# Kernel optimization log

Measured on AMD Instinct MI355X. Metric: run time of the kernel, lower is better.

## Reference

```python
import jax, jax.numpy as jnp
import numpy as np

D_IN = 2048
D_OUT = 2048
NUM_HEADS = 16
HEAD_DIM = D_OUT // NUM_HEADS


def setup_inputs() -> dict:
    key = jax.random.key(0)
    k_x, k_qkv, k_proj, k_b = jax.random.split(key, 4)
    x = jax.random.normal(k_x, (2, 2048, D_IN), dtype=jnp.float32)
    # torch Linear(d_in, 3*d_out, bias=False): weight [3*d_out, d_in]; store transposed [d_in, 3*d_out]
    Wqkv = jax.random.normal(k_qkv, (D_IN, 3 * D_OUT), dtype=jnp.float32) / np.sqrt(D_IN)
    Wproj = jax.random.normal(k_proj, (D_OUT, D_OUT), dtype=jnp.float32) / np.sqrt(D_OUT)
    bproj = jax.random.normal(k_b, (D_OUT,), dtype=jnp.float32) * 0.01
    return {"x": x, "Wqkv": Wqkv, "Wproj": Wproj, "bproj": bproj}


def reference(x, Wqkv, Wproj, bproj):
    B, S, _ = x.shape
    qkv = x @ Wqkv  # [B, S, 3*D_OUT]
    qkv = qkv.reshape(B, S, 3, NUM_HEADS, HEAD_DIM)
    qkv = jnp.transpose(qkv, (2, 0, 3, 1, 4))  # [3, B, H, S, Dh]
    q, k, v = qkv[0], qkv[1], qkv[2]
    scale = 1.0 / np.sqrt(HEAD_DIM).astype(np.float32)
    scores = jnp.einsum('bhqd,bhkd->bhqk', q, k) * scale  # [B, H, S, S]
    causal = jnp.tril(jnp.ones((S, S), dtype=bool))
    scores = jnp.where(causal, scores, jnp.finfo(scores.dtype).min)
    attn = jax.nn.softmax(scores, axis=-1)
    out = jnp.einsum('bhqk,bhkd->bhqd', attn, v)  # [B, H, S, Dh]
    out = jnp.transpose(out, (0, 2, 1, 3)).reshape(B, S, D_OUT)
    return out @ Wproj + bproj
```

## Files before the change

### kernel.cpp

```cpp
#include <hip/hip_runtime.h>
#include <stdint.h>

typedef __attribute__((ext_vector_type(8))) short short8;
typedef __attribute__((ext_vector_type(4))) float f32x4;
typedef __attribute__((ext_vector_type(16))) float f32x16;
typedef __attribute__((ext_vector_type(4))) unsigned short u16x4;

typedef unsigned short u16;

constexpr int S_LEN = 2048;
constexpr int DH    = 128;

__device__ __forceinline__ u16 f2bf(float f) {
    union { float f; unsigned u; } v; v.f = f;
    unsigned r = v.u + 0x7FFFu + ((v.u >> 16) & 1u);
    return (u16)(r >> 16);
}
__device__ __forceinline__ void gl_lds16(const void* g, void* l) {
    __builtin_amdgcn_global_load_lds((const __attribute__((address_space(1))) void*)g,
                                     (__attribute__((address_space(3))) void*)l,
                                     16, 0, 0);
}

__global__ __launch_bounds__(256) void convx(const float* __restrict__ src,
                                             u16* __restrict__ dst) {
    size_t i = ((size_t)blockIdx.x * 256 + threadIdx.x) * 8;
    f32x4 a = *(const f32x4*)(src + i);
    f32x4 b = *(const f32x4*)(src + i + 4);
    short8 r;
    r[0] = (short)f2bf(a[0]); r[1] = (short)f2bf(a[1]);
    r[2] = (short)f2bf(a[2]); r[3] = (short)f2bf(a[3]);
    r[4] = (short)f2bf(b[0]); r[5] = (short)f2bf(b[1]);
    r[6] = (short)f2bf(b[2]); r[7] = (short)f2bf(b[3]);
    *(short8*)(dst + i) = r;
}

__global__ __launch_bounds__(256) void convT(const float* __restrict__ src,
                                             u16* __restrict__ dst,
                                             int rows, int cols) {
    __shared__ u16 t[64][65];
    const int c0 = blockIdx.x * 64, r0 = blockIdx.y * 64;
    const int tid = threadIdx.x;
    const int colq = (tid & 15) * 4;
    const int rw   = tid >> 4;
#pragma unroll
    for (int p = 0; p < 4; ++p) {
        int row = p * 16 + rw;
        f32x4 v = *(const f32x4*)(src + (size_t)(r0 + row) * cols + c0 + colq);
        t[colq + 0][row] = f2bf(v[0]);
        t[colq + 1][row] = f2bf(v[1]);
        t[colq + 2][row] = f2bf(v[2]);
        t[colq + 3][row] = f2bf(v[3]);
    }
    __syncthreads();
    const int rowq = (tid & 15) * 4;
    const int cw   = tid >> 4;
#pragma unroll
    for (int p = 0; p < 4; ++p) {
        int col = p * 16 + cw;
        u16x4 o;
        o[0] = t[col][rowq + 0]; o[1] = t[col][rowq + 1];
        o[2] = t[col][rowq + 2]; o[3] = t[col][rowq + 3];
        *(u16x4*)(dst + (size_t)(c0 + col) * rows + r0 + rowq) = o;
    }
}

__global__ __launch_bounds__(512, 2) void gemm_qkv(
        const u16* __restrict__ A, const u16* __restrict__ BT,
        u16* __restrict__ Qo, u16* __restrict__ Ko, u16* __restrict__ VTo) {
    __shared__ __align__(16) u16 lA[2][128 * 64];
    __shared__ __align__(16) u16 lB[2][256 * 64];
    const int tid = threadIdx.x;
    const int lane = tid & 63, wave = tid >> 6;
    const int quad = lane >> 4, l16 = lane & 15;
    const int wr = wave >> 2, wc = wave & 3;
    const int m0 = blockIdx.y * 128, n0 = blockIdx.x * 256;
    const int sw = l16 & 7;
    const int c4 = tid & 7;
    f32x4 acc[4][4] = {};

    auto stageA = [&](int t1, int nb) {
#pragma unroll
        for (int j = 0; j < 2; ++j) {
            int idx = j * 512 + tid;
            int row = idx >> 3;
            gl_lds16(A + (size_t)(m0 + row) * 2048 + t1 * 64 + ((c4 ^ (row & 7)) * 8),
                     &lA[nb][row * 64 + c4 * 8]);
        }
    };
    auto stageB = [&](int h, int t1, int nb) {
#pragma unroll
        for (int j = 0; j < 2; ++j) {
            int rih = (j * 512 + tid) >> 3;
            int row = (rih & 31) + h * 32 + (rih >> 5) * 64;
            gl_lds16(BT + (size_t)(n0 + row) * 2048 + t1 * 64 + ((c4 ^ (row & 7)) * 8),
                     &lB[nb][row * 64 + c4 * 8]);
        }
    };

    stageA(0, 0); stageB(0, 0, 0); stageB(1, 0, 0);

    constexpr int NT = 32;
    for (int t = 0; t < NT; ++t) {
        const int buf = t & 1, nb = buf ^ 1;
        const bool pf = (t + 1 < NT);
        asm volatile("s_waitcnt vmcnt(2)\n\ts_barrier" ::: "memory");
        short8 af[4][2], bf0[2][2];
        const int abase = (wr * 64 + l16) * 64;
        const int bbase = (wc * 64 + l16) * 64;
#pragma unroll
        for (int m = 0; m < 4; ++m)
#pragma unroll
            for (int ks = 0; ks < 2; ++ks)
                af[m][ks] = *(const short8*)&lA[buf][abase + m * 1024 + (((ks * 4 + quad) ^ sw)) * 8];
#pragma unroll
        for (int n = 0; n < 2; ++n)
#pragma unroll
            for (int ks = 0; ks < 2; ++ks)
                bf0[n][ks] = *(const short8*)&lB[buf][bbase + n * 1024 + (((ks * 4 + quad) ^ sw)) * 8];
        if (pf) { stageA(t + 1, nb); stageB(0, t + 1, nb); }
        __builtin_amdgcn_s_setprio(1);
#pragma unroll
        for (int m = 0; m < 4; ++m)
#pragma unroll
            for (int n = 0; n < 2; ++n)
#pragma unroll
                for (int ks = 0; ks < 2; ++ks)
                    acc[m][n] = __builtin_amdgcn_mfma_f32_16x16x32_bf16(
                        af[m][ks], bf0[n][ks], acc[m][n], 0, 0, 0);
        __builtin_amdgcn_s_setprio(0);
        if (pf) asm volatile("s_waitcnt vmcnt(4)\n\ts_barrier" ::: "memory");
        else    asm volatile("s_waitcnt vmcnt(0)\n\ts_barrier" ::: "memory");
        short8 bf1[2][2];
#pragma unroll
        for (int n = 0; n < 2; ++n)
#pragma unroll
            for (int ks = 0; ks < 2; ++ks)
                bf1[n][ks] = *(const short8*)&lB[buf][bbase + 2048 + n * 1024 + (((ks * 4 + quad) ^ sw)) * 8];
        if (pf) stageB(1, t + 1, nb);
        __builtin_amdgcn_s_setprio(1);
#pragma unroll
        for (int m = 0; m < 4; ++m)
#pragma unroll
            for (int n = 0; n < 2; ++n)
#pragma unroll
                for (int ks = 0; ks < 2; ++ks)
                    acc[m][n + 2] = __builtin_amdgcn_mfma_f32_16x16x32_bf16(
                        af[m][ks], bf1[n][ks], acc[m][n + 2], 0, 0, 0);
        __builtin_amdgcn_s_setprio(0);
    }

#pragma unroll
    for (int m = 0; m < 4; ++m) {
        int r0r = m0 + wr * 64 + m * 16 + quad * 4;
        int b = r0r >> 11, s0 = r0r & 2047;
#pragma unroll
        for (int n = 0; n < 4; ++n) {
            int cc = n0 + wc * 64 + n * 16 + l16;
            int which = cc >> 11, hd = (cc >> 7) & 15, dh = cc & 127;
            if (which < 2) {
                u16* dst = which == 0 ? Qo : Ko;
#pragma unroll
                for (int rg = 0; rg < 4; ++rg)
                    dst[(size_t)((b * 16 + hd) * 2048 + s0 + rg) * 128 + dh] = f2bf(acc[m][n][rg]);
            } else {
                u16x4 v;
#pragma unroll
                for (int rg = 0; rg < 4; ++rg) v[rg] = f2bf(acc[m][n][rg]);
                *(u16x4*)&VTo[((size_t)(b * 16 + hd) * 128 + dh) * 2048 + s0] = v;
            }
        }
    }
}

__global__ __launch_bounds__(256, 2) void attn_kern(
        u16* __restrict__ QOp, const u16* __restrict__ Kp,
        const u16* __restrict__ VTp) {
    __shared__ __align__(16) u16 lK[2][64 * 128];
    __shared__ __align__(16) u16 lV[2][128 * 64];
    const int tid = threadIdx.x, lane = tid & 63, wave = tid >> 6;
    const int ql = lane & 31, hi = lane >> 5;
    const int qb = (blockIdx.y < 8) ? (15 - (int)blockIdx.y) : ((int)blockIdx.y - 8);
    const int bh = blockIdx.x;
    const int qbase = qb * 128 + wave * 32;
    const int qmax = qbase + 31;
    const int nkt = 2 * qb + 2;
    u16* Qh = QOp + (size_t)bh * S_LEN * DH;
    const u16* Kh = Kp + (size_t)bh * S_LEN * DH;
    const u16* VTh = VTp + (size_t)bh * DH * S_LEN;

    short8 qf[8];
#pragma unroll
    for (int c = 0; c < 8; ++c)
        qf[c] = *(const short8*)&Qh[(size_t)(qbase + ql) * 128 + c * 16 + hi * 8];

    f32x16 acc[4] = {};
    float mrun = -1e30f, lrun = 0.f;
    const float SC = 0.08838834764831845f * 1.44269504088896f;

    auto stageK = [&](int kt, int b) {
        const u16* ks = Kh + (size_t)kt * 64 * 128;
#pragma unroll
        for (int p = 0; p < 4; ++p) {
            int slot = p * 256 + tid;
            int row = slot >> 4, c4 = slot & 15;
            gl_lds16(ks + row * 128 + ((c4 ^ (row & 15)) * 8), &lK[b][slot * 8]);
        }
    };
    auto stageV = [&](int kt, int b) {
        const u16* vs = VTh + kt * 64;
#pragma unroll
        for (int p = 0; p < 4; ++p) {
            int slot = p * 256 + tid;
            int row = slot >> 3, c4 = slot & 7;
            gl_lds16(vs + (size_t)row * 2048 + ((c4 ^ (row & 7)) * 8), &lV[b][slot * 8]);
        }
    };

    stageK(0, 0);
    stageV(0, 0);
    asm volatile("s_waitcnt vmcnt(4)\n\ts_barrier" ::: "memory");

    for (int kt = 0; kt < nkt; ++kt) {
        const int buf = kt & 1;
        const bool more = kt + 1 < nkt;
        const bool compute = (kt * 64 <= qmax);
        float pv0[16], pv1[16];
        if (compute) {
            const bool part = (kt * 64 + 63 > qbase);
            f32x16 s0 = {}, s1 = {};
            __builtin_amdgcn_s_setprio(1);
#pragma unroll
            for (int c = 0; c < 8; ++c) {
                int sl = ((c * 2 + hi) ^ (ql & 15)) * 8;
                short8 k0 = *(const short8*)&lK[buf][ql * 128 + sl];
                short8 k1 = *(const short8*)&lK[buf][(32 + ql) * 128 + sl];
                s0 = __builtin_amdgcn_mfma_f32_32x32x16_bf16(k0, qf[c], s0, 0, 0, 0);
                s1 = __builtin_amdgcn_mfma_f32_32x32x16_bf16(k1, qf[c], s1, 0, 0, 0);
            }
            __builtin_amdgcn_s_setprio(0);
            if (more) stageK(kt + 1, buf ^ 1);
            float pm = -1e30f;
            const int qg = qbase + ql;
#pragma unroll
            for (int r = 0; r < 16; ++r) {
                int krow = (r & 3) + 8 * (r >> 2) + 4 * hi;
                float a = s0[r] * SC;
                float b = s1[r] * SC;
                if (part) {
                    if (kt * 64 + krow > qg)      a = -1e30f;
                    if (kt * 64 + 32 + krow > qg) b = -1e30f;
                }
                pv0[r] = a; pv1[r] = b;
                pm = fmaxf(pm, fmaxf(a, b));
            }
            pm = fmaxf(pm, __shfl_xor(pm, 32));
            if (__any(pm - mrun > 8.f)) {
                float mn = fmaxf(mrun, pm);
                float al = exp2f(mrun - mn);
                mrun = mn;
                lrun *= al;
#pragma unroll
                for (int r = 0; r < 16; ++r) {
                    float ar = __shfl(al, (r & 3) + 8 * (r >> 2) + 4 * hi);
#pragma unroll
                    for (int dc = 0; dc < 4; ++dc)
                        acc[dc][r] *= ar;
                }
            }
            float rs = 0.f;
#pragma unroll
            for (int r = 0; r < 16; ++r) {
                pv0[r] = exp2f(pv0[r] - mrun);
                pv1[r] = exp2f(pv1[r] - mrun);
                rs += pv0[r] + pv1[r];
            }
            rs += __shfl_xor(rs, 32);
            lrun += rs;
        } else if (more) {
            stageK(kt + 1, buf ^ 1);
        }
        if (more) asm volatile("s_waitcnt vmcnt(4)\n\ts_barrier" ::: "memory");
        else      asm volatile("s_waitcnt vmcnt(0)\n\ts_barrier" ::: "memory");
        if (compute) {
            unsigned X0[8], X1[8];
#pragma unroll
            for (int i = 0; i < 8; ++i) {
                X0[i] = (unsigned)f2bf(pv0[2 * i]) | ((unsigned)f2bf(pv0[2 * i + 1]) << 16);
                X1[i] = (unsigned)f2bf(pv1[2 * i]) | ((unsigned)f2bf(pv1[2 * i + 1]) << 16);
            }
            short8 pa[4];
#pragma unroll
            for (int t = 0; t < 2; ++t)
#pragma unroll
                for (int h = 0; h < 2; ++h) {
                    unsigned x0 = t ? X1[4 * h + 0] : X0[4 * h + 0];
                    unsigned x1 = t ? X1[4 * h + 1] : X0[4 * h + 1];
                    unsigned x2 = t ? X1[4 * h + 2] : X0[4 * h + 2];
                    unsigned x3 = t ? X1[4 * h + 3] : X0[4 * h + 3];
                    unsigned sx0 = (unsigned)__shfl_xor((int)x0, 32);
                    unsigned sx1 = (unsigned)__shfl_xor((int)x1, 32);
                    unsigned sx2 = (unsigned)__shfl_xor((int)x2, 32);
                    unsigned sx3 = (unsigned)__shfl_xor((int)x3, 32);
                    union { unsigned u[4]; short8 s; } uf;
                    uf.u[0] = hi ? sx2 : x0;
                    uf.u[1] = hi ? sx3 : x1;
                    uf.u[2] = hi ? x2 : sx0;
                    uf.u[3] = hi ? x3 : sx1;
                    pa[t * 2 + h] = uf.s;
                }
            __builtin_amdgcn_s_setprio(1);
#pragma unroll
            for (int dc = 0; dc < 4; ++dc) {
                const int rv = dc * 32 + ql;
#pragma unroll
                for (int kc = 0; kc < 4; ++kc) {
                    short8 vf = *(const short8*)&lV[buf][rv * 64 + (((kc * 2 + hi) ^ (ql & 7)) * 8)];
                    acc[dc] = __builtin_amdgcn_mfma_f32_32x32x16_bf16(pa[kc], vf, acc[dc], 0, 0, 0);
                }
            }
            __builtin_amdgcn_s_setprio(0);
        }
        if (more) {
            stageV(kt + 1, buf ^ 1);
            asm volatile("s_waitcnt vmcnt(4)\n\ts_barrier" ::: "memory");
        }
    }

    float linv = 1.f / lrun;
#pragma unroll
    for (int r = 0; r < 16; ++r) {
        int qr = (r & 3) + 8 * (r >> 2) + 4 * hi;
        float lr = __shfl(linv, qr);
        int qq = qbase + qr;
#pragma unroll
        for (int dc = 0; dc < 4; ++dc)
            Qh[(size_t)qq * 128 + dc * 32 + ql] = f2bf(acc[dc][r] * lr);
    }
}

__global__ __launch_bounds__(256, 2) void gemm_proj(
        const u16* __restrict__ QO, const u16* __restrict__ BT,
        const float* __restrict__ bias, float* __restrict__ out) {
    __shared__ __align__(16) u16 lA[2][128 * 64];
    __shared__ __align__(16) u16 lB[2][128 * 64];
    const int tid = threadIdx.x;
    const int lane = tid & 63, wave = tid >> 6;
    const int quad = lane >> 4, l16 = lane & 15;
    const int wm = wave >> 1, wn = wave & 1;
    const int bid = blockIdx.x;
    const int swz = (bid & 7) * 64 + (bid >> 3);
    const int m0 = (swz >> 4) * 128, n0 = (swz & 15) * 128;
    const int sw = l16 & 7;
    const int c4 = tid & 7;
    f32x4 acc[4][4] = {};

    auto stageA = [&](int t1, int nb) {
#pragma unroll
        for (int j = 0; j < 4; ++j) {
            int row = (j * 256 + tid) >> 3;
            int r = m0 + row;
            int b = r >> 11, s = r & 2047;
            int k = t1 * 64 + ((c4 ^ (row & 7)) * 8);
            int h = k >> 7, dh = k & 127;
            gl_lds16(QO + ((size_t)(b * 16 + h) * 2048 + s) * 128 + dh,
                     &lA[nb][row * 64 + c4 * 8]);
        }
    };
    auto stageB = [&](int h, int t1, int nb) {
#pragma unroll
        for (int j = 0; j < 2; ++j) {
            int rih = (j * 256 + tid) >> 3;
            int row = (rih & 31) + h * 32 + (rih >> 5) * 64;
            gl_lds16(BT + (size_t)(n0 + row) * 2048 + t1 * 64 + ((c4 ^ (row & 7)) * 8),
                     &lB[nb][row * 64 + c4 * 8]);
        }
    };

    stageB(0, 0, 0);
    asm volatile("" ::: "memory");
    stageA(0, 0);
    asm volatile("" ::: "memory");
    stageB(1, 0, 0);

    constexpr int NT = 32;
    for (int t = 0; t < NT; ++t) {
        const int buf = t & 1, nb = buf ^ 1;
        const bool pf = (t + 1 < NT);
        asm volatile("s_waitcnt vmcnt(2)\n\ts_barrier" ::: "memory");
        short8 af[4][2], bf0[2][2];
        const int abase = (wm * 64 + l16) * 64;
        const int bbase = (wn * 64 + l16) * 64;
#pragma unroll
        for (int m = 0; m < 4; ++m)
#pragma unroll
            for (int ks = 0; ks < 2; ++ks)
                af[m][ks] = *(const short8*)&lA[buf][abase + m * 1024 + (((ks * 4 + quad) ^ sw)) * 8];
#pragma unroll
        for (int n = 0; n < 2; ++n)
#pragma unroll
            for (int ks = 0; ks < 2; ++ks)
                bf0[n][ks] = *(const short8*)&lB[buf][bbase + n * 1024 + (((ks * 4 + quad) ^ sw)) * 8];
        if (pf) {
            stageB(0, t + 1, nb);
            asm volatile("" ::: "memory");
            stageA(t + 1, nb);
        }
        __builtin_amdgcn_s_setprio(1);
#pragma unroll
        for (int m = 0; m < 4; ++m)
#pragma unroll
            for (int n = 0; n < 2; ++n)
#pragma unroll
                for (int ks = 0; ks < 2; ++ks)
                    acc[m][n] = __builtin_amdgcn_mfma_f32_16x16x32_bf16(
                        af[m][ks], bf0[n][ks], acc[m][n], 0, 0, 0);
        __builtin_amdgcn_s_setprio(0);
        if (pf) asm volatile("s_waitcnt vmcnt(6)\n\ts_barrier" ::: "memory");
        else    asm volatile("s_waitcnt vmcnt(0)\n\ts_barrier" ::: "memory");
        short8 bf1[2][2];
#pragma unroll
        for (int n = 0; n < 2; ++n)
#pragma unroll
            for (int ks = 0; ks < 2; ++ks)
                bf1[n][ks] = *(const short8*)&lB[buf][bbase + 2048 + n * 1024 + (((ks * 4 + quad) ^ sw)) * 8];
        if (pf) stageB(1, t + 1, nb);
        __builtin_amdgcn_s_setprio(1);
#pragma unroll
        for (int m = 0; m < 4; ++m)
#pragma unroll
            for (int n = 0; n < 2; ++n)
#pragma unroll
                for (int ks = 0; ks < 2; ++ks)
                    acc[m][n + 2] = __builtin_amdgcn_mfma_f32_16x16x32_bf16(
                        af[m][ks], bf1[n][ks], acc[m][n + 2], 0, 0, 0);
        __builtin_amdgcn_s_setprio(0);
    }

#pragma unroll
    for (int m = 0; m < 4; ++m) {
        int r0r = m0 + wm * 64 + m * 16 + quad * 4;
#pragma unroll
        for (int n = 0; n < 4; ++n) {
            int cc = n0 + wn * 64 + n * 16 + l16;
            float bv = bias[cc];
#pragma unroll
            for (int rg = 0; rg < 4; ++rg)
                out[(size_t)(r0r + rg) * 2048 + cc] = acc[m][n][rg] + bv;
        }
    }
}

extern "C" void kernel_launch(void* const* d_in, const int* in_sizes, int n_in,
                              void* d_out, int out_size, void* d_ws, size_t ws_size,
                              hipStream_t stream) {
    const float *x = nullptr, *Wqkv = nullptr, *Wproj = nullptr, *bproj = nullptr;
    for (int i = 0; i < n_in; ++i) {
        int sz = in_sizes[i];
        if      (sz == 2 * 2048 * 2048) x     = (const float*)d_in[i];
        else if (sz == 2048 * 6144)     Wqkv  = (const float*)d_in[i];
        else if (sz == 2048 * 2048)     Wproj = (const float*)d_in[i];
        else if (sz == 2048)            bproj = (const float*)d_in[i];
    }
    float* out = (float*)d_out;

    u16* xb     = (u16*)d_ws;
    u16* WqkvT  = xb    + (size_t)4096 * 2048;
    u16* Qb     = WqkvT + (size_t)6144 * 2048;
    u16* Kb     = Qb    + (size_t)32 * 2048 * 128;
    u16* VTb    = Kb    + (size_t)32 * 2048 * 128;
    u16* WprojT = xb;

    convx<<<dim3(4096), dim3(256), 0, stream>>>(x, xb);
    convT<<<dim3(96, 32), dim3(256), 0, stream>>>(Wqkv, WqkvT, 2048, 6144);
    gemm_qkv<<<dim3(24, 32), dim3(512), 0, stream>>>(xb, WqkvT, Qb, Kb, VTb);
    convT<<<dim3(32, 32), dim3(256), 0, stream>>>(Wproj, WprojT, 2048, 2048);
    attn_kern<<<dim3(32, 16), dim3(256), 0, stream>>>(Qb, Kb, VTb);
    gemm_proj<<<dim3(512), dim3(256), 0, stream>>>(Qb, WprojT, bproj, out);
}
```

Before: 371.3 us.

## Merge weight transposes into one launch, split mask path, use packed bf16 convert

The two weight transpose-convert kernels become a single launch that covers both matrices, and WprojT moves to its own workspace region so it no longer aliases xb. In the attention kernel, the score scaling loop is split into a masked and an unmasked branch, and the P-to-bf16 packing uses the hardware v_cvt_pk_bf16_f32 instruction in place of manual rounding. The attention grid is also remapped to (qblock, bh) with plain ordering, which drops the heavy-first ordering of causal blocks and may worsen load balance. The workspace footprint grows, and the hardware convert's rounding may differ slightly from the manual round-to-nearest-even.

Measured after the change: 376.0 us. About the same (+1.3%).

```diff
diff --git a/kernel.cpp b/kernel.cpp
--- a/kernel.cpp
+++ b/kernel.cpp
@@ -15,6 +15,11 @@
     union { float f; unsigned u; } v; v.f = f;
     unsigned r = v.u + 0x7FFFu + ((v.u >> 16) & 1u);
     return (u16)(r >> 16);
+}
+__device__ __forceinline__ unsigned cvt_pk_bf16(float lo, float hi) {
+    unsigned r;
+    asm("v_cvt_pk_bf16_f32 %0, %1, %2" : "=v"(r) : "v"(lo), "v"(hi));
+    return r;
 }
 __device__ __forceinline__ void gl_lds16(const void* g, void* l) {
     __builtin_amdgcn_global_load_lds((const __attribute__((address_space(1))) void*)g,
@@ -35,11 +40,19 @@
     *(short8*)(dst + i) = r;
 }
 
-__global__ __launch_bounds__(256) void convT(const float* __restrict__ src,
-                                             u16* __restrict__ dst,
-                                             int rows, int cols) {
+__global__ __launch_bounds__(256) void convT2(const float* __restrict__ s1,
+                                              u16* __restrict__ d1,
+                                              const float* __restrict__ s2,
+                                              u16* __restrict__ d2) {
     __shared__ u16 t[64][65];
-    const int c0 = blockIdx.x * 64, r0 = blockIdx.y * 64;
+    const int bx = blockIdx.x;
+    const bool first = bx < 96;
+    const float* src = first ? s1 : s2;
+    u16* dst = first ? d1 : d2;
+    const int cols = first ? 6144 : 2048;
+    const int c0 = (first ? bx : bx - 96) * 64;
+    const int r0 = blockIdx.y * 64;
+    const int rows = 2048;
     const int tid = threadIdx.x;
     const int colq = (tid & 15) * 4;
     const int rw   = tid >> 4;
@@ -180,8 +193,8 @@
     __shared__ __align__(16) u16 lV[2][128 * 64];
     const int tid = threadIdx.x, lane = tid & 63, wave = tid >> 6;
     const int ql = lane & 31, hi = lane >> 5;
-    const int qb = (blockIdx.y < 8) ? (15 - (int)blockIdx.y) : ((int)blockIdx.y - 8);
-    const int bh = blockIdx.x;
+    const int qb = blockIdx.x;
+    const int bh = blockIdx.y;
     const int qbase = qb * 128 + wave * 32;
     const int qmax = qbase + 31;
     const int nkt = 2 * qb + 2;
@@ -242,17 +255,25 @@
             if (more) stageK(kt + 1, buf ^ 1);
             float pm = -1e30f;
             const int qg = qbase + ql;
-#pragma unroll
-            for (int r = 0; r < 16; ++r) {
-                int krow = (r & 3) + 8 * (r >> 2) + 4 * hi;
-                float a = s0[r] * SC;
-                float b = s1[r] * SC;
-                if (part) {
+            if (part) {
+#pragma unroll
+                for (int r = 0; r < 16; ++r) {
+                    int krow = (r & 3) + 8 * (r >> 2) + 4 * hi;
+                    float a = s0[r] * SC;
+                    float b = s1[r] * SC;
                     if (kt * 64 + krow > qg)      a = -1e30f;
                     if (kt * 64 + 32 + krow > qg) b = -1e30f;
+                    pv0[r] = a; pv1[r] = b;
+                    pm = fmaxf(pm, fmaxf(a, b));
                 }
-                pv0[r] = a; pv1[r] = b;
-                pm = fmaxf(pm, fmaxf(a, b));
+            } else {
+#pragma unroll
+                for (int r = 0; r < 16; ++r) {
+                    float a = s0[r] * SC;
+                    float b = s1[r] * SC;
+                    pv0[r] = a; pv1[r] = b;
+                    pm = fmaxf(pm, fmaxf(a, b));
+                }
             }
             pm = fmaxf(pm, __shfl_xor(pm, 32));
             if (__any(pm - mrun > 8.f)) {
@@ -286,8 +307,8 @@
             unsigned X0[8], X1[8];
 #pragma unroll
             for (int i = 0; i < 8; ++i) {
-                X0[i] = (unsigned)f2bf(pv0[2 * i]) | ((unsigned)f2bf(pv0[2 * i + 1]) << 16);
-                X1[i] = (unsigned)f2bf(pv1[2 * i]) | ((unsigned)f2bf(pv1[2 * i + 1]) << 16);
+                X0[i] = cvt_pk_bf16(pv0[2 * i], pv0[2 * i + 1]);
+                X1[i] = cvt_pk_bf16(pv1[2 * i], pv1[2 * i + 1]);
             }
             short8 pa[4];
 #pragma unroll
@@ -469,12 +490,11 @@
     u16* Qb     = WqkvT + (size_t)6144 * 2048;
     u16* Kb     = Qb    + (size_t)32 * 2048 * 128;
     u16* VTb    = Kb    + (size_t)32 * 2048 * 128;
-    u16* WprojT = xb;
+    u16* WprojT = VTb   + (size_t)32 * 2048 * 128;
 
     convx<<<dim3(4096), dim3(256), 0, stream>>>(x, xb);
-    convT<<<dim3(96, 32), dim3(256), 0, stream>>>(Wqkv, WqkvT, 2048, 6144);
+    convT2<<<dim3(128, 32), dim3(256), 0, stream>>>(Wqkv, WqkvT, Wproj, WprojT);
     gemm_qkv<<<dim3(24, 32), dim3(512), 0, stream>>>(xb, WqkvT, Qb, Kb, VTb);
-    convT<<<dim3(32, 32), dim3(256), 0, stream>>>(Wproj, WprojT, 2048, 2048);
-    attn_kern<<<dim3(32, 16), dim3(256), 0, stream>>>(Qb, Kb, VTb);
+    attn_kern<<<dim3(16, 32), dim3(256), 0, stream>>>(Qb, Kb, VTb);
     gemm_proj<<<dim3(512), dim3(256), 0, stream>>>(Qb, WprojT, bproj, out);
 }
```
